# Kernel optimization log

Hardware: AMD Instinct MI355X
Metric: run time of the kernel (lower is better)

Reference implementation:

```python
import jax, jax.numpy as jnp
import numpy as np

NP_, NA, EC, EW = 50000, 100000, 300000, 500000
PD, AD, ED, HD, NI = 768, 128, 768, 64, 3
FUSED = HD * 2 + ED + 1  # 897


def _lin_init(k, fan_in, shape):
    s = 1.0 / np.sqrt(fan_in)
    return jax.random.uniform(k, shape, minval=-s, maxval=s, dtype=jnp.float32)


def setup_inputs() -> dict:
    key = jax.random.key(0)
    ks = jax.random.split(key, 30)
    inp = {
        'x_paper': jax.random.normal(ks[0], (NP_, PD), dtype=jnp.float32),
        'x_author': jax.random.normal(ks[1], (NA, AD), dtype=jnp.float32),
        'cites_edge_index': jax.random.randint(ks[2], (2, EC), 0, NP_, dtype=jnp.int32),
        'writes_src': jax.random.randint(ks[3], (EW,), 0, NA, dtype=jnp.int32),
        'writes_dst': jax.random.randint(ks[4], (EW,), 0, NP_, dtype=jnp.int32),
        'cites_edge_attr': jax.random.normal(ks[5], (EC, ED), dtype=jnp.float32),
        'delta_t': jax.random.uniform(ks[6], (EC, 1), dtype=jnp.float32),
        # projections
        'W_pp': _lin_init(ks[7], PD, (PD, HD)), 'b_pp': jnp.zeros((HD,), jnp.float32),
        'W_ap': _lin_init(ks[8], AD, (AD, HD)), 'b_ap': jnp.zeros((HD,), jnp.float32),
        # TemporalGATConv params
        'Wq': _lin_init(ks[9], HD, (HD, HD)), 'bq': jnp.zeros((HD,), jnp.float32),
        'Wk': _lin_init(ks[10], HD, (HD, HD)), 'bk': jnp.zeros((HD,), jnp.float32),
        'Wv': _lin_init(ks[11], HD, (HD, HD)), 'bv': jnp.zeros((HD,), jnp.float32),
        'We': _lin_init(ks[12], ED, (ED, HD)), 'be': jnp.zeros((HD,), jnp.float32),
        'lam': jnp.float32(0.1),
        # SAGEConv params (mean aggr; lin_l on aggregated, lin_r on root, no bias on lin_r)
        'sage_Wl': _lin_init(ks[13], HD, (HD, HD)), 'sage_bl': jnp.zeros((HD,), jnp.float32),
        'sage_Wr': _lin_init(ks[14], HD, (HD, HD)),
        # intent head
        'W_head': _lin_init(ks[15], FUSED, (FUSED, NI)), 'b_head': jnp.zeros((NI,), jnp.float32),
    }
    return inp


def reference(x_paper, x_author, cites_edge_index, writes_src, writes_dst,
              cites_edge_attr, delta_t,
              W_pp, b_pp, W_ap, b_ap,
              Wq, bq, Wk, bk, Wv, bv, We, be, lam,
              sage_Wl, sage_bl, sage_Wr, W_head, b_head):
    xp = jax.nn.relu(x_paper @ W_pp + b_pp)    # [NP, HD]
    xa = jax.nn.relu(x_author @ W_ap + b_ap)   # [NA, HD]

    # --- SAGEConv (author -> paper), mean aggregation ---
    agg = jax.ops.segment_sum(xa[writes_src], writes_dst, num_segments=NP_)
    deg = jax.ops.segment_sum(jnp.ones((EW,), jnp.float32), writes_dst, num_segments=NP_)
    mean_nb = agg / jnp.maximum(deg, 1.0)[:, None]
    h_sage = mean_nb @ sage_Wl + sage_bl + xp @ sage_Wr

    # --- TemporalGATConv (paper -cites-> paper) ---
    q = xp @ Wq + bq
    k = xp @ Wk + bk
    v = xp @ Wv + bv
    src, dst = cites_edge_index[0], cites_edge_index[1]
    e_feat = cites_edge_attr @ We + be                         # [EC, HD]
    alpha = jnp.sum(q[dst] * k[src] * e_feat, axis=-1) / np.sqrt(HD).astype(np.float32)
    decay = jnp.exp(-jnp.abs(lam) * delta_t[:, 0])
    alpha = alpha * decay
    # segment softmax over destination neighborhoods
    m = jax.ops.segment_max(alpha, dst, num_segments=NP_)
    ex = jnp.exp(alpha - m[dst])
    denom = jax.ops.segment_sum(ex, dst, num_segments=NP_)
    alpha = ex / (denom[dst] + 1e-16)
    h_gat = jax.ops.segment_sum(v[src] * alpha[:, None], dst, num_segments=NP_)

    # HeteroConv aggr='sum' over edge types targeting 'paper'
    h_papers = jax.nn.relu(h_sage + h_gat)

    # edge representation + intent head (dropout is identity in eval)
    edge_rep = jnp.concatenate([h_papers[src], h_papers[dst], cites_edge_attr, delta_t], axis=-1)
    intent_logits = edge_rep @ W_head + b_head
    return intent_logits, alpha
```

## Files before the change

kernel.cpp:

```cpp
#include <hip/hip_runtime.h>
#include <hip/hip_bf16.h>

#define NP_ 50000
#define NA_ 100000
#define EC_ 300000
#define EW_ 500000
#define PD_ 768
#define AD_ 128
#define ED_ 768
#define HD_ 64

template <int KK>
__global__ __launch_bounds__(256) void proj_relu_kernel(
    const float* __restrict__ X, const float* __restrict__ W,
    const float* __restrict__ b, float* __restrict__ out) {
  __shared__ float xs[16][KK];
  const int t = threadIdx.x;
  const size_t row_base = (size_t)blockIdx.x * 16;

  const float4* s4 = (const float4*)(X + row_base * KK);
  float4* d4 = (float4*)&xs[0][0];
  const int nvec = 16 * KK / 4;
  for (int vI = t; vI < nvec; vI += 256) d4[vI] = s4[vI];
  __syncthreads();

  const int n = t & 63, w = t >> 6;
  float acc[4] = {0.f, 0.f, 0.f, 0.f};
  for (int k = 0; k < KK; k += 4) {
    const float w0 = W[(k + 0) * 64 + n];
    const float w1 = W[(k + 1) * 64 + n];
    const float w2 = W[(k + 2) * 64 + n];
    const float w3 = W[(k + 3) * 64 + n];
#pragma unroll
    for (int i = 0; i < 4; ++i) {
      const float4 x4 = *(const float4*)&xs[w * 4 + i][k];
      acc[i] += x4.x * w0 + x4.y * w1 + x4.z * w2 + x4.w * w3;
    }
  }
  const float bn = b[n];
#pragma unroll
  for (int i = 0; i < 4; ++i) {
    const size_t row = row_base + w * 4 + i;
    out[row * 64 + n] = fmaxf(acc[i] + bn, 0.f);
  }
}

__global__ __launch_bounds__(256) void sage_scatter_kernel(
    const float* __restrict__ xa, const int* __restrict__ wsrc,
    const int* __restrict__ wdst, float* __restrict__ agg,
    float* __restrict__ deg) {
  const int tid = blockIdx.x * 256 + threadIdx.x;
  const int e = tid >> 6, n = tid & 63;
  const int s = wsrc[e], d = wdst[e];
  atomicAdd(&agg[(size_t)d * 64 + n], xa[(size_t)s * 64 + n]);
  if (n == 0) atomicAdd(&deg[d], 1.0f);
}

__global__ __launch_bounds__(256) void sage_qkv_kernel(
    const float* __restrict__ xp, const float* __restrict__ agg,
    const float* __restrict__ deg, const float* __restrict__ Wl,
    const float* __restrict__ bl, const float* __restrict__ Wr,
    const float* __restrict__ Wq, const float* __restrict__ bq,
    const float* __restrict__ Wk, const float* __restrict__ bk,
    const float* __restrict__ Wv, const float* __restrict__ bv,
    float* __restrict__ h_sage, float* __restrict__ qo,
    float* __restrict__ ko, float* __restrict__ vo) {
  __shared__ float xs[16][64];
  __shared__ float ms[16][64];
  const int t = threadIdx.x;
  const size_t row_base = (size_t)blockIdx.x * 16;
  {
    const float4* a4 = (const float4*)(agg + row_base * 64);
    const float4* x4 = (const float4*)(xp + row_base * 64);
    const int i = t >> 4;
    const float rd = 1.0f / fmaxf(deg[row_base + i], 1.0f);
    float4 av = a4[t];
    av.x *= rd; av.y *= rd; av.z *= rd; av.w *= rd;
    ((float4*)&ms[0][0])[t] = av;
    ((float4*)&xs[0][0])[t] = x4[t];
  }
  __syncthreads();
  const int n = t & 63, w = t >> 6;
  float hs[4] = {0, 0, 0, 0}, aq[4] = {0, 0, 0, 0};
  float ak[4] = {0, 0, 0, 0}, av_[4] = {0, 0, 0, 0};
  for (int kk = 0; kk < 64; ++kk) {
    const float wl = Wl[kk * 64 + n];
    const float wr = Wr[kk * 64 + n];
    const float wq = Wq[kk * 64 + n];
    const float wk = Wk[kk * 64 + n];
    const float wv = Wv[kk * 64 + n];
#pragma unroll
    for (int i = 0; i < 4; ++i) {
      const float xv = xs[w * 4 + i][kk];
      const float mv = ms[w * 4 + i][kk];
      hs[i] += mv * wl + xv * wr;
      aq[i] += xv * wq;
      ak[i] += xv * wk;
      av_[i] += xv * wv;
    }
  }
  const float bln = bl[n], bqn = bq[n], bkn = bk[n], bvn = bv[n];
#pragma unroll
  for (int i = 0; i < 4; ++i) {
    const size_t row = row_base + w * 4 + i;
    h_sage[row * 64 + n] = hs[i] + bln;
    qo[row * 64 + n] = aq[i] + bqn;
    ko[row * 64 + n] = ak[i] + bkn;
    vo[row * 64 + n] = av_[i] + bvn;
  }
}

__global__ __launch_bounds__(256) void edge_kernel(
    const float* __restrict__ attr, const float* __restrict__ We,
    const float* __restrict__ be, const float* __restrict__ q,
    const float* __restrict__ kmat, const int* __restrict__ src,
    const int* __restrict__ dst, const float* __restrict__ dt,
    const float* __restrict__ lam_p, const float* __restrict__ Wh,
    float* __restrict__ ex_buf, float* __restrict__ denom,
    float* __restrict__ head_attr) {
  __shared__ float as_[16][768];
  __shared__ float ps[4][16][64];
  const int t = threadIdx.x;
  const int n = t & 63, w = t >> 6;
  const size_t e_base = (size_t)blockIdx.x * 16;

  const float4* s4 = (const float4*)(attr + e_base * 768);
  float4* d4 = (float4*)&as_[0][0];
  for (int vI = t; vI < 3072; vI += 256) d4[vI] = s4[vI];
  __syncthreads();

  float acc[16];
#pragma unroll
  for (int e = 0; e < 16; ++e) acc[e] = 0.f;
  const int k0 = 192 * w;
  for (int kk = k0; kk < k0 + 192; kk += 4) {
    const float w0 = We[(kk + 0) * 64 + n];
    const float w1 = We[(kk + 1) * 64 + n];
    const float w2 = We[(kk + 2) * 64 + n];
    const float w3 = We[(kk + 3) * 64 + n];
#pragma unroll
    for (int e = 0; e < 16; ++e) {
      const float4 a4 = *(const float4*)&as_[e][kk];
      acc[e] += a4.x * w0 + a4.y * w1 + a4.z * w2 + a4.w * w3;
    }
  }
#pragma unroll
  for (int e = 0; e < 16; ++e) ps[w][e][n] = acc[e];
  __syncthreads();

  const float lam = fabsf(lam_p[0]);
#pragma unroll
  for (int i = 0; i < 4; ++i) {
    const int el = 4 * w + i;
    const size_t eg = e_base + el;
    const float ef = ps[0][el][n] + ps[1][el][n] + ps[2][el][n] +
                     ps[3][el][n] + be[n];
    const int sp = src[eg], dp = dst[eg];
    float tv = q[(size_t)dp * 64 + n] * kmat[(size_t)sp * 64 + n] * ef;
#pragma unroll
    for (int off = 32; off; off >>= 1) tv += __shfl_xor(tv, off);
    const float alpha = tv * 0.125f * expf(-lam * dt[eg]);
    const float exv = expf(alpha);
    if (n == 0) {
      ex_buf[eg] = exv;
      atomicAdd(&denom[dp], exv);
    }
  }

#pragma unroll
  for (int i = 0; i < 4; ++i) {
    const int el = 4 * w + i;
    const size_t eg = e_base + el;
#pragma unroll
    for (int j = 0; j < 3; ++j) {
      float p = 0.f;
      for (int kk = n; kk < 768; kk += 64) p += as_[el][kk] * Wh[(128 + kk) * 3 + j];
#pragma unroll
      for (int off = 32; off; off >>= 1) p += __shfl_xor(p, off);
      if (n == 0) head_attr[eg * 3 + j] = p + dt[eg] * Wh[896 * 3 + j];
    }
  }
}

__global__ __launch_bounds__(256) void gat_scatter_kernel(
    const float* __restrict__ v, const int* __restrict__ src,
    const int* __restrict__ dst, const float* __restrict__ ex_buf,
    const float* __restrict__ denom, float* __restrict__ h_gat,
    float* __restrict__ alpha_out) {
  const int tid = blockIdx.x * 256 + threadIdx.x;
  const int e = tid >> 6, n = tid & 63;
  const int sp = src[e], dp = dst[e];
  const float wgt = ex_buf[e] / (denom[dp] + 1e-16f);
  atomicAdd(&h_gat[(size_t)dp * 64 + n], wgt * v[(size_t)sp * 64 + n]);
  if (n == 0) alpha_out[e] = wgt;
}

__global__ __launch_bounds__(256) void paper_head_kernel(
    const float* __restrict__ h_sage, const float* __restrict__ h_gat,
    const float* __restrict__ Wh, float* __restrict__ c_src,
    float* __restrict__ c_dst) {
  const int t = threadIdx.x, n = t & 63, w = t >> 6;
  const size_t p = (size_t)blockIdx.x * 4 + w;
  const float val = fmaxf(h_sage[p * 64 + n] + h_gat[p * 64 + n], 0.f);
  float r[6];
#pragma unroll
  for (int j = 0; j < 3; ++j) {
    r[j] = val * Wh[n * 3 + j];
    r[3 + j] = val * Wh[(64 + n) * 3 + j];
  }
#pragma unroll
  for (int j = 0; j < 6; ++j) {
#pragma unroll
    for (int off = 32; off; off >>= 1) r[j] += __shfl_xor(r[j], off);
  }
  if (n == 0) {
#pragma unroll
    for (int j = 0; j < 3; ++j) {
      c_src[p * 3 + j] = r[j];
      c_dst[p * 3 + j] = r[3 + j];
    }
  }
}

__global__ __launch_bounds__(256) void edge_head_kernel(
    const int* __restrict__ src, const int* __restrict__ dst,
    const float* __restrict__ c_src, const float* __restrict__ c_dst,
    const float* __restrict__ head_attr, const float* __restrict__ bh,
    float* __restrict__ logits) {
  const int e = blockIdx.x * 256 + threadIdx.x;
  if (e >= EC_) return;
  const int sp = src[e], dp = dst[e];
#pragma unroll
  for (int j = 0; j < 3; ++j) {
    logits[(size_t)e * 3 + j] = c_src[(size_t)sp * 3 + j] +
                                c_dst[(size_t)dp * 3 + j] +
                                head_attr[(size_t)e * 3 + j] + bh[j];
  }
}

extern "C" void kernel_launch(void* const* d_in, const int* in_sizes, int n_in,
                              void* d_out, int out_size, void* d_ws,
                              size_t ws_size, hipStream_t stream) {
  const float* x_paper = (const float*)d_in[0];
  const float* x_author = (const float*)d_in[1];
  const int* cei = (const int*)d_in[2];
  const int* wsrc = (const int*)d_in[3];
  const int* wdst = (const int*)d_in[4];
  const float* attr = (const float*)d_in[5];
  const float* dt = (const float*)d_in[6];
  const float* W_pp = (const float*)d_in[7];
  const float* b_pp = (const float*)d_in[8];
  const float* W_ap = (const float*)d_in[9];
  const float* b_ap = (const float*)d_in[10];
  const float* Wq = (const float*)d_in[11];
  const float* bq = (const float*)d_in[12];
  const float* Wk = (const float*)d_in[13];
  const float* bk = (const float*)d_in[14];
  const float* Wv = (const float*)d_in[15];
  const float* bv = (const float*)d_in[16];
  const float* We = (const float*)d_in[17];
  const float* be = (const float*)d_in[18];
  const float* lam = (const float*)d_in[19];
  const float* sage_Wl = (const float*)d_in[20];
  const float* sage_bl = (const float*)d_in[21];
  const float* sage_Wr = (const float*)d_in[22];
  const float* W_head = (const float*)d_in[23];
  const float* b_head = (const float*)d_in[24];

  const int* src = cei;
  const int* dstp = cei + EC_;

  float* ws = (float*)d_ws;
  float* xa = ws;
  float* xp = xa + (size_t)NA_ * 64;
  float* agg = xp + (size_t)NP_ * 64;
  float* deg = agg + (size_t)NP_ * 64;
  float* denom = deg + NP_;
  float* h_gat = denom + NP_;
  float* h_sage = h_gat + (size_t)NP_ * 64;
  float* q = h_sage + (size_t)NP_ * 64;
  float* k = q + (size_t)NP_ * 64;
  float* v = k + (size_t)NP_ * 64;
  float* ex_buf = v + (size_t)NP_ * 64;
  float* head_attr = ex_buf + EC_;
  float* c_src = head_attr + (size_t)EC_ * 3;
  float* c_dst = c_src + (size_t)NP_ * 3;

  hipMemsetAsync(agg, 0, (size_t)(NP_ * 64 + NP_ + NP_ + NP_ * 64) * sizeof(float), stream);

  float* logits = (float*)d_out;
  float* alpha_out = logits + (size_t)EC_ * 3;

  proj_relu_kernel<128><<<NA_ / 16, 256, 0, stream>>>(x_author, W_ap, b_ap, xa);
  sage_scatter_kernel<<<EW_ * 64 / 256, 256, 0, stream>>>(xa, wsrc, wdst, agg, deg);
  proj_relu_kernel<768><<<NP_ / 16, 256, 0, stream>>>(x_paper, W_pp, b_pp, xp);
  sage_qkv_kernel<<<NP_ / 16, 256, 0, stream>>>(xp, agg, deg, sage_Wl, sage_bl,
                                                sage_Wr, Wq, bq, Wk, bk, Wv, bv,
                                                h_sage, q, k, v);
  edge_kernel<<<EC_ / 16, 256, 0, stream>>>(attr, We, be, q, k, src, dstp, dt,
                                            lam, W_head, ex_buf, denom, head_attr);
  gat_scatter_kernel<<<EC_ * 64 / 256, 256, 0, stream>>>(v, src, dstp, ex_buf,
                                                         denom, h_gat, alpha_out);
  paper_head_kernel<<<NP_ / 4, 256, 0, stream>>>(h_sage, h_gat, W_head, c_src, c_dst);
  edge_head_kernel<<<(EC_ + 255) / 256, 256, 0, stream>>>(src, dstp, c_src, c_dst,
                                                          head_attr, b_head, logits);
}
```

Before: 3.293 ms.

## Chunk edge attribute staging through smaller LDS tile to raise edge_kernel occupancy

```diff
diff --git a/kernel.cpp b/kernel.cpp
--- a/kernel.cpp
+++ b/kernel.cpp
@@ -110,7 +110,7 @@
   }
 }
 
-__global__ __launch_bounds__(256) void edge_kernel(
+__global__ __launch_bounds__(256, 6) void edge_kernel(
     const float* __restrict__ attr, const float* __restrict__ We,
     const float* __restrict__ be, const float* __restrict__ q,
     const float* __restrict__ kmat, const int* __restrict__ src,
@@ -118,34 +118,63 @@
     const float* __restrict__ lam_p, const float* __restrict__ Wh,
     float* __restrict__ ex_buf, float* __restrict__ denom,
     float* __restrict__ head_attr) {
-  __shared__ float as_[16][768];
-  __shared__ float ps[4][16][64];
+  __shared__ float as_[16][256];
+  __shared__ float ps[2][16][64];
   const int t = threadIdx.x;
   const int n = t & 63, w = t >> 6;
   const size_t e_base = (size_t)blockIdx.x * 16;
 
-  const float4* s4 = (const float4*)(attr + e_base * 768);
-  float4* d4 = (float4*)&as_[0][0];
-  for (int vI = t; vI < 3072; vI += 256) d4[vI] = s4[vI];
-  __syncthreads();
-
-  float acc[16];
-#pragma unroll
-  for (int e = 0; e < 16; ++e) acc[e] = 0.f;
-  const int k0 = 192 * w;
-  for (int kk = k0; kk < k0 + 192; kk += 4) {
-    const float w0 = We[(kk + 0) * 64 + n];
-    const float w1 = We[(kk + 1) * 64 + n];
-    const float w2 = We[(kk + 2) * 64 + n];
-    const float w3 = We[(kk + 3) * 64 + n];
-#pragma unroll
-    for (int e = 0; e < 16; ++e) {
-      const float4 a4 = *(const float4*)&as_[e][kk];
-      acc[e] += a4.x * w0 + a4.y * w1 + a4.z * w2 + a4.w * w3;
-    }
-  }
-#pragma unroll
-  for (int e = 0; e < 16; ++e) ps[w][e][n] = acc[e];
+  const int eg8 = (w >> 1) * 8;
+  const int kh = (w & 1) * 128;
+  const float* WhA = Wh + 128 * 3;
+
+  float acc[8];
+#pragma unroll
+  for (int i = 0; i < 8; ++i) acc[i] = 0.f;
+  float hp[4][3];
+#pragma unroll
+  for (int i = 0; i < 4; ++i) hp[i][0] = hp[i][1] = hp[i][2] = 0.f;
+
+  for (int c = 0; c < 3; ++c) {
+    const int ck0 = c << 8;
+    if (c) __syncthreads();
+    for (int vI = t; vI < 1024; vI += 256) {
+      const int r = vI >> 6, c4 = vI & 63;
+      ((float4*)&as_[r][0])[c4] =
+          ((const float4*)(attr + (e_base + r) * 768 + ck0))[c4];
+    }
+    __syncthreads();
+
+    for (int kk = kh; kk < kh + 128; kk += 4) {
+      const int gk = ck0 + kk;
+      const float w0 = We[(gk + 0) * 64 + n];
+      const float w1 = We[(gk + 1) * 64 + n];
+      const float w2 = We[(gk + 2) * 64 + n];
+      const float w3 = We[(gk + 3) * 64 + n];
+#pragma unroll
+      for (int i = 0; i < 8; ++i) {
+        const float4 a4 = *(const float4*)&as_[eg8 + i][kk];
+        acc[i] += a4.x * w0 + a4.y * w1 + a4.z * w2 + a4.w * w3;
+      }
+    }
+
+#pragma unroll
+    for (int kt = 0; kt < 4; ++kt) {
+      const int k = n + kt * 64;
+      const float* whr = WhA + (size_t)(ck0 + k) * 3;
+      const float wh0 = whr[0], wh1 = whr[1], wh2 = whr[2];
+#pragma unroll
+      for (int i = 0; i < 4; ++i) {
+        const float av = as_[4 * w + i][k];
+        hp[i][0] += av * wh0;
+        hp[i][1] += av * wh1;
+        hp[i][2] += av * wh2;
+      }
+    }
+  }
+
+#pragma unroll
+  for (int i = 0; i < 8; ++i) ps[w & 1][eg8 + i][n] = acc[i];
   __syncthreads();
 
   const float lam = fabsf(lam_p[0]);
@@ -153,8 +182,7 @@
   for (int i = 0; i < 4; ++i) {
     const int el = 4 * w + i;
     const size_t eg = e_base + el;
-    const float ef = ps[0][el][n] + ps[1][el][n] + ps[2][el][n] +
-                     ps[3][el][n] + be[n];
+    const float ef = ps[0][el][n] + ps[1][el][n] + be[n];
     const int sp = src[eg], dp = dst[eg];
     float tv = q[(size_t)dp * 64 + n] * kmat[(size_t)sp * 64 + n] * ef;
 #pragma unroll
@@ -169,12 +197,10 @@
 
 #pragma unroll
   for (int i = 0; i < 4; ++i) {
-    const int el = 4 * w + i;
-    const size_t eg = e_base + el;
+    const size_t eg = e_base + 4 * w + i;
 #pragma unroll
     for (int j = 0; j < 3; ++j) {
-      float p = 0.f;
-      for (int kk = n; kk < 768; kk += 64) p += as_[el][kk] * Wh[(128 + kk) * 3 + j];
+      float p = hp[i][j];
 #pragma unroll
       for (int off = 32; off; off >>= 1) p += __shfl_xor(p, off);
       if (n == 0) head_attr[eg * 3 + j] = p + dt[eg] * Wh[896 * 3 + j];
```

Result: faster. 2.783 ms (-15.5%).
